# Optimization experiments

Hardware: AMD Instinct MI355X
Metric: run time of the kernel (lower is better)

## Reference

```python
import jax, jax.numpy as jnp
import numpy as np

N_FREQ = 12
NUM_LODS = 8
NUM_SAMPLED_LODS = 1
N_NEURONS = 64
OUT_CH = 11  # NUM_CANONICAL_CHANNELS = sum([3,3,1,1,1,1,1])
LRELU_SLOPE = 0.01
B = 1 << 20
# base_res = max_resolution >> (n_levels - 1); fpl = save_bits // quantize_bits = 4
GRIDS = [dict(base_res=16, n_levels=8, fpl=4),   # max_res 2048
         dict(base_res=16, n_levels=7, fpl=4)]   # max_res 1024


def _level_geom(base_res, level):
    # tcnn dense grid: scale = base_res * 2^level - 1, res = ceil(scale) + 1
    scale = base_res * (2.0 ** level) - 1.0
    res = int(np.ceil(scale)) + 1
    return res, scale


def _grid_n_params(g):
    return sum(_level_geom(g['base_res'], l)[0] ** 2 for l in range(g['n_levels'])) * g['fpl']


def triangle_wave(uv, n_freq):
    # tcnn TriangleWave: per dim, per frequency f: tri(x * 2^f), dim-major layout
    freqs = (2.0 ** jnp.arange(n_freq, dtype=jnp.float32))
    xf = uv[:, :, None] * freqs                      # [B, 2, F]
    t = jnp.abs(xf - jnp.floor(xf + 0.5)) * 4.0 - 1.0
    return t.reshape(uv.shape[0], -1)                # [B, 2*F]


def dense_grid_encode(uv, params_flat, base_res, n_levels, fpl):
    # Multi-level dense grid with bilinear interpolation (tcnn Grid/Dense/Linear).
    feats = []
    offset = 0
    for level in range(n_levels):
        res, scale = _level_geom(base_res, level)
        n = res * res * fpl
        table = params_flat[offset:offset + n].reshape(res * res, fpl)
        offset += n
        pos = uv * scale + 0.5                       # [B, 2]
        p0f = jnp.floor(pos)
        w = pos - p0f                                # bilinear weights
        p0 = jnp.clip(p0f.astype(jnp.int32), 0, res - 1)
        p1 = jnp.minimum(p0 + 1, res - 1)
        ix0, iy0 = p0[:, 0], p0[:, 1]
        ix1, iy1 = p1[:, 0], p1[:, 1]
        # tcnn index stride: dim0 fastest -> idx = ix + iy*res
        f00 = table[iy0 * res + ix0]
        f10 = table[iy0 * res + ix1]
        f01 = table[iy1 * res + ix0]
        f11 = table[iy1 * res + ix1]
        wx = w[:, 0:1]
        wy = w[:, 1:2]
        f = (f00 * (1 - wx) + f10 * wx) * (1 - wy) + (f01 * (1 - wx) + f11 * wx) * wy
        feats.append(f)                              # [B, fpl]
    return jnp.concatenate(feats, axis=1)            # [B, n_levels*fpl], level-major


def _forward(x, grid0_params, grid1_params, W_in, W_h, W_out):
    uvs = jnp.remainder(x[:, 0:2], 1.0)
    lod = x[:, 2:3]
    mips = lod * (NUM_LODS - NUM_SAMPLED_LODS)       # [B, 1]
    pe = triangle_wave(uvs, N_FREQ)                  # [B, 24]
    feats = []
    for g, params in zip(GRIDS, [grid0_params, grid1_params]):
        L, F = g['n_levels'], g['fpl']
        allf = dense_grid_encode(uvs, params, g['base_res'], L, F)  # [B, L*F]
        clipped = jnp.minimum(mips, float(L - NUM_SAMPLED_LODS))
        cols = ((L - NUM_SAMPLED_LODS - clipped) * F
                + jnp.arange(F * NUM_SAMPLED_LODS, dtype=jnp.float32)).astype(jnp.int32)
        feats.append(jnp.take_along_axis(allf, cols, axis=1))       # [B, F]
    inp = jnp.concatenate([pe] + feats + [lod], axis=1)             # [B, 33]
    lrelu = lambda h: jnp.where(h > 0, h, LRELU_SLOPE * h)
    h = lrelu(inp @ W_in)
    h = lrelu(h @ W_h)
    return lrelu(h @ W_out)                          # [B, 11]


def setup_inputs() -> dict:
    key = jax.random.key(0)
    ks = jax.random.split(key, 6)
    x = jax.random.uniform(ks[0], (B, 3), dtype=jnp.float32)
    grid0 = jax.random.uniform(ks[1], (_grid_n_params(GRIDS[0]),), jnp.float32, -0.1, 0.1)
    grid1 = jax.random.uniform(ks[2], (_grid_n_params(GRIDS[1]),), jnp.float32, -0.1, 0.1)
    n_in = N_FREQ * 2 + sum(g['fpl'] for g in GRIDS) * NUM_SAMPLED_LODS + 1
    W_in = jax.random.normal(ks[3], (n_in, N_NEURONS), jnp.float32) / np.float32(np.sqrt(n_in))
    W_h = jax.random.normal(ks[4], (N_NEURONS, N_NEURONS), jnp.float32) / np.float32(np.sqrt(N_NEURONS))
    W_out = jax.random.normal(ks[5], (N_NEURONS, OUT_CH), jnp.float32) / np.float32(np.sqrt(N_NEURONS))
    return dict(x=x, grid0_params=grid0, grid1_params=grid1, W_in=W_in, W_h=W_h, W_out=W_out)


def reference(x, grid0_params, grid1_params, W_in, W_h, W_out):
    return _forward(x, grid0_params, grid1_params, W_in, W_h, W_out)
```

## Files before the change

### kernel.cpp

```cpp
#include <hip/hip_runtime.h>

typedef float f32x4 __attribute__((ext_vector_type(4)));
typedef __bf16 bf16x8 __attribute__((ext_vector_type(8)));

#define PERM __builtin_amdgcn_perm

static __device__ __forceinline__ bf16x8 as_bf(uint4 v) {
    union { uint4 u; bf16x8 b; } c; c.u = v; return c.b;
}

static __device__ __forceinline__ float lrelu(float x) { return x > 0.0f ? x : 0.01f * x; }

static __device__ __forceinline__ unsigned pack_hilo(float v) {
    unsigned b = __float_as_uint(v);
    unsigned hi = (b + 0x7FFFu + ((b >> 16) & 1u)) >> 16;
    float hif = __uint_as_float(hi << 16);
    float lof = v - hif;
    unsigned lb = __float_as_uint(lof);
    unsigned lo = (lb + 0x7FFFu + ((lb >> 16) & 1u)) >> 16;
    return (hi << 16) | lo;
}

static __device__ __forceinline__ void unpack_frag(uint4 p0, uint4 p1, uint4& hi, uint4& lo) {
    hi.x = PERM(p0.y, p0.x, 0x07060302u);
    hi.y = PERM(p0.w, p0.z, 0x07060302u);
    hi.z = PERM(p1.y, p1.x, 0x07060302u);
    hi.w = PERM(p1.w, p1.z, 0x07060302u);
    lo.x = PERM(p0.y, p0.x, 0x05040100u);
    lo.y = PERM(p0.w, p0.z, 0x05040100u);
    lo.z = PERM(p1.y, p1.x, 0x05040100u);
    lo.w = PERM(p1.w, p1.z, 0x05040100u);
}

static __device__ __forceinline__ void read_frag_w(const unsigned* q, uint4& hi, uint4& lo) {
    uint4 p0 = *(const uint4*)(q);
    uint4 p1 = *(const uint4*)(q + 4);
    unpack_frag(p0, p1, hi, lo);
}

static __device__ __forceinline__ void read_frag_a(const unsigned* actb, int r, int kbase, int g,
                                                   uint4& hi, uint4& lo) {
    const unsigned* row = actb + r * 64;
    int cb = (kbase >> 2) + 2 * g;
    int rx = r & 15;
    uint4 p0 = *(const uint4*)(row + ((cb ^ rx) << 2));
    uint4 p1 = *(const uint4*)(row + (((cb + 1) ^ rx) << 2));
    unpack_frag(p0, p1, hi, lo);
}

static __device__ __forceinline__ void act_store(unsigned* actb, int row, int col, unsigned val) {
    int pos = row * 64 + ((((col >> 2) ^ (row & 15)) << 2) | (col & 3));
    actb[pos] = val;
}

static __device__ __forceinline__ f32x4 mfma3(const uint4& ah, const uint4& al,
                                              const uint4& bh, const uint4& bl, f32x4 c) {
    c = __builtin_amdgcn_mfma_f32_16x16x32_bf16(as_bf(ah), as_bf(bh), c, 0, 0, 0);
    c = __builtin_amdgcn_mfma_f32_16x16x32_bf16(as_bf(al), as_bf(bh), c, 0, 0, 0);
    c = __builtin_amdgcn_mfma_f32_16x16x32_bf16(as_bf(ah), as_bf(bl), c, 0, 0, 0);
    return c;
}

static __device__ __forceinline__ void bilerp(const float4* __restrict__ tbl, float u, float v,
                                              int l, float out[4]) {
    const int res = 16 << l;
    const float scale = (float)(res - 1);
    float px = u * scale + 0.5f;
    float py = v * scale + 0.5f;
    float fx = floorf(px), fy = floorf(py);
    float wx = px - fx, wy = py - fy;
    int ix0 = min(max((int)fx, 0), res - 1);
    int iy0 = min(max((int)fy, 0), res - 1);
    int ix1 = min(ix0 + 1, res - 1);
    int iy1 = min(iy0 + 1, res - 1);
    unsigned base = (0x55555555u & ((1u << (2 * l)) - 1u)) * 256u;
    float4 f00 = tbl[base + iy0 * res + ix0];
    float4 f10 = tbl[base + iy0 * res + ix1];
    float4 f01 = tbl[base + iy1 * res + ix0];
    float4 f11 = tbl[base + iy1 * res + ix1];
    float owx = 1.0f - wx, owy = 1.0f - wy;
    out[0] = (f00.x * owx + f10.x * wx) * owy + (f01.x * owx + f11.x * wx) * wy;
    out[1] = (f00.y * owx + f10.y * wx) * owy + (f01.y * owx + f11.y * wx) * wy;
    out[2] = (f00.z * owx + f10.z * wx) * owy + (f01.z * owx + f11.z * wx) * wy;
    out[3] = (f00.w * owx + f10.w * wx) * owy + (f01.w * owx + f11.w * wx) * wy;
}

static __device__ __forceinline__ void grid_select(const float4* __restrict__ tbl, float u, float v,
                                                   float mips, float Lm1, float out[4]) {
    float clipped = fminf(mips, Lm1);
    float c0 = (Lm1 - clipped) * 4.0f;
    asm volatile("" : "+v"(c0));
    int col0 = (int)c0;
    int col1 = (int)(c0 + 1.0f);
    int col2 = (int)(c0 + 2.0f);
    int col3 = (int)(c0 + 3.0f);
    int lA = col0 >> 2;
    int lB = col3 >> 2;
    float A[4], Bv[4];
    bilerp(tbl, u, v, lA, A);
    bilerp(tbl, u, v, lB, Bv);
    int cols[4] = {col0, col1, col2, col3};
    #pragma unroll
    for (int j = 0; j < 4; ++j) {
        int lj = cols[j] >> 2;
        int fj = cols[j] & 3;
        float va = A[0];
        va = (fj == 1) ? A[1] : va;
        va = (fj == 2) ? A[2] : va;
        va = (fj == 3) ? A[3] : va;
        float vb = Bv[0];
        vb = (fj == 1) ? Bv[1] : vb;
        vb = (fj == 2) ? Bv[2] : vb;
        vb = (fj == 3) ? Bv[3] : vb;
        out[j] = (lj == lA) ? va : vb;
    }
}

#define LDS_U32 (2048 + 4096 + 1024 + 64 + 128 + 8192)

__global__ __launch_bounds__(256, 2) void tcnn_fwd(
    const float* __restrict__ x,
    const float4* __restrict__ g0,
    const float4* __restrict__ g1,
    const float* __restrict__ Win,
    const float* __restrict__ Wh,
    const float* __restrict__ Wout,
    float* __restrict__ out,
    int npts)
{
    extern __shared__ unsigned smem[];
    unsigned* s_winT  = smem;
    unsigned* s_whT   = s_winT + 2048;
    unsigned* s_woutT = s_whT + 4096;
    float*    s_lodw  = (float*)(s_woutT + 1024);
    float*    s_lodv  = s_lodw + 64;
    unsigned* s_act   = (unsigned*)(s_lodv + 128);

    const int tid = threadIdx.x;

    for (int e = tid; e < 2048; e += 256) {
        int n = e >> 5, k = e & 31;
        s_winT[n * 32 + k] = pack_hilo(Win[k * 64 + n]);
    }
    for (int e = tid; e < 4096; e += 256) {
        int n = e >> 6, k = e & 63;
        s_whT[n * 64 + k] = pack_hilo(Wh[k * 64 + n]);
    }
    for (int e = tid; e < 1024; e += 256) {
        int n = e >> 6, k = e & 63;
        float w = (n < 11) ? Wout[k * 11 + n] : 0.0f;
        s_woutT[n * 64 + k] = pack_hilo(w);
    }
    if (tid < 64) s_lodw[tid] = Win[32 * 64 + tid];
    __syncthreads();

    const int wv = tid >> 6;
    const int l = tid & 63;
    const int g = l >> 4;
    const int m = l & 15;
    const int half = l >> 5;
    const int p = l & 31;

    unsigned* act = s_act + wv * 2048;
    float* lodv = s_lodv + wv * 32;

    uint4 w1h[4], w1l[4];
    #pragma unroll
    for (int Nt = 0; Nt < 4; ++Nt)
        read_frag_w(s_winT + (Nt * 16 + m) * 32 + 8 * g, w1h[Nt], w1l[Nt]);
    uint4 w2h[4][2], w2l[4][2];
    #pragma unroll
    for (int Nt = 0; Nt < 4; ++Nt)
        #pragma unroll
        for (int ks = 0; ks < 2; ++ks)
            read_frag_w(s_whT + (Nt * 16 + m) * 64 + ks * 32 + 8 * g, w2h[Nt][ks], w2l[Nt][ks]);
    uint4 w3h[2], w3l[2];
    #pragma unroll
    for (int ks = 0; ks < 2; ++ks)
        read_frag_w(s_woutT + m * 64 + ks * 32 + 8 * g, w3h[ks], w3l[ks]);

    for (int cb = (blockIdx.x * 4 + wv) * 32; cb + 31 < npts; cb += gridDim.x * 128) {
        int gp = cb + p;
        float xu = x[gp * 3 + 0];
        float xv = x[gp * 3 + 1];
        float xl = x[gp * 3 + 2];
        float u = xu - floorf(xu);
        float vv = xv - floorf(xv);
        float coord = half ? vv : u;
        #pragma unroll
        for (int f = 0; f < 12; ++f) {
            float fr = (float)(1 << f);
            float xf = coord * fr;
            float t = fabsf(xf - floorf(xf + 0.5f)) * 4.0f - 1.0f;
            act_store(act, p, half * 12 + f, pack_hilo(t));
        }
        {
            const float4* tbl = half ? g1 : g0;
            float Lm1 = half ? 6.0f : 7.0f;
            float mips = xl * 7.0f;
            float gf[4];
            grid_select(tbl, u, vv, mips, Lm1, gf);
            #pragma unroll
            for (int j = 0; j < 4; ++j)
                act_store(act, p, 24 + half * 4 + j, pack_hilo(gf[j]));
        }
        if (half) lodv[p] = xl;
        __builtin_amdgcn_wave_barrier();

        uint4 a1h[2], a1l[2];
        #pragma unroll
        for (int Mt = 0; Mt < 2; ++Mt)
            read_frag_a(act, Mt * 16 + m, 0, g, a1h[Mt], a1l[Mt]);
        f32x4 acc1[2][4];
        #pragma unroll
        for (int Mt = 0; Mt < 2; ++Mt)
            #pragma unroll
            for (int Nt = 0; Nt < 4; ++Nt)
                acc1[Mt][Nt] = (f32x4){0.f, 0.f, 0.f, 0.f};
        #pragma unroll
        for (int Nt = 0; Nt < 4; ++Nt)
            #pragma unroll
            for (int Mt = 0; Mt < 2; ++Mt)
                acc1[Mt][Nt] = mfma3(a1h[Mt], a1l[Mt], w1h[Nt], w1l[Nt], acc1[Mt][Nt]);
        float lv[2][4];
        #pragma unroll
        for (int Mt = 0; Mt < 2; ++Mt)
            #pragma unroll
            for (int i = 0; i < 4; ++i)
                lv[Mt][i] = lodv[Mt * 16 + 4 * g + i];
        #pragma unroll
        for (int Nt = 0; Nt < 4; ++Nt) {
            float wl = s_lodw[Nt * 16 + m];
            #pragma unroll
            for (int Mt = 0; Mt < 2; ++Mt)
                #pragma unroll
                for (int i = 0; i < 4; ++i)
                    acc1[Mt][Nt][i] = fmaf(lv[Mt][i], wl, acc1[Mt][Nt][i]);
        }
        __builtin_amdgcn_wave_barrier();
        #pragma unroll
        for (int Mt = 0; Mt < 2; ++Mt)
            #pragma unroll
            for (int Nt = 0; Nt < 4; ++Nt)
                #pragma unroll
                for (int i = 0; i < 4; ++i)
                    act_store(act, Mt * 16 + 4 * g + i, Nt * 16 + m,
                              pack_hilo(lrelu(acc1[Mt][Nt][i])));
        __builtin_amdgcn_wave_barrier();

        f32x4 acc2[2][4];
        #pragma unroll
        for (int Mt = 0; Mt < 2; ++Mt)
            #pragma unroll
            for (int Nt = 0; Nt < 4; ++Nt)
                acc2[Mt][Nt] = (f32x4){0.f, 0.f, 0.f, 0.f};
        #pragma unroll
        for (int Mt = 0; Mt < 2; ++Mt) {
            uint4 ah[2], al[2];
            #pragma unroll
            for (int ks = 0; ks < 2; ++ks)
                read_frag_a(act, Mt * 16 + m, ks * 32, g, ah[ks], al[ks]);
            #pragma unroll
            for (int Nt = 0; Nt < 4; ++Nt)
                #pragma unroll
                for (int ks = 0; ks < 2; ++ks)
                    acc2[Mt][Nt] = mfma3(ah[ks], al[ks], w2h[Nt][ks], w2l[Nt][ks], acc2[Mt][Nt]);
        }
        __builtin_amdgcn_wave_barrier();
        #pragma unroll
        for (int Mt = 0; Mt < 2; ++Mt)
            #pragma unroll
            for (int Nt = 0; Nt < 4; ++Nt)
                #pragma unroll
                for (int i = 0; i < 4; ++i)
                    act_store(act, Mt * 16 + 4 * g + i, Nt * 16 + m,
                              pack_hilo(lrelu(acc2[Mt][Nt][i])));
        __builtin_amdgcn_wave_barrier();

        f32x4 acc3[2];
        acc3[0] = (f32x4){0.f, 0.f, 0.f, 0.f};
        acc3[1] = (f32x4){0.f, 0.f, 0.f, 0.f};
        #pragma unroll
        for (int Mt = 0; Mt < 2; ++Mt) {
            uint4 ah[2], al[2];
            #pragma unroll
            for (int ks = 0; ks < 2; ++ks)
                read_frag_a(act, Mt * 16 + m, ks * 32, g, ah[ks], al[ks]);
            #pragma unroll
            for (int ks = 0; ks < 2; ++ks)
                acc3[Mt] = mfma3(ah[ks], al[ks], w3h[ks], w3l[ks], acc3[Mt]);
        }
        #pragma unroll
        for (int Mt = 0; Mt < 2; ++Mt)
            #pragma unroll
            for (int i = 0; i < 4; ++i) {
                int row = Mt * 16 + 4 * g + i;
                float val = lrelu(acc3[Mt][i]);
                if (m < 11) out[(size_t)(cb + row) * 11 + m] = val;
            }
        __builtin_amdgcn_wave_barrier();
    }
}

extern "C" void kernel_launch(void* const* d_in, const int* in_sizes, int n_in,
                              void* d_out, int out_size, void* d_ws, size_t ws_size,
                              hipStream_t stream) {
    const float* x = (const float*)d_in[0];
    const float4* g0 = (const float4*)d_in[1];
    const float4* g1 = (const float4*)d_in[2];
    const float* Win = (const float*)d_in[3];
    const float* Wh = (const float*)d_in[4];
    const float* Wout = (const float*)d_in[5];
    float* out = (float*)d_out;
    int npts = in_sizes[0] / 3;
    tcnn_fwd<<<512, 256, LDS_U32 * 4, stream>>>(x, g0, g1, Win, Wh, Wout, out, npts);
}
```

Before: 275.7 us.

## Software-pipeline grid gathers for next tile behind current tile's MLP MFMAs

Splits the grid lookup into an issue phase (load eight float4 table entries) and a finish phase (bilinear blend). Inside the persistent loop, the x loads, gathers and positional encoding for the next 32-point tile are issued after the first MFMA layer of the current tile and consumed at the end of the iteration. This hides gather latency behind the matrix work. In exchange, the eight float4s and the packed features stay live across the MLP, raising register pressure under the 2-blocks-per-SM launch bound.

New measurement: 306.4 us. +11.1%, slower.

```diff
diff --git a/kernel.cpp b/kernel.cpp
--- a/kernel.cpp
+++ b/kernel.cpp
@@ -61,45 +61,59 @@
     return c;
 }
 
-static __device__ __forceinline__ void bilerp(const float4* __restrict__ tbl, float u, float v,
-                                              int l, float out[4]) {
+static __device__ __forceinline__ void issue_level(const float4* __restrict__ tbl, float u, float v,
+                                                   int l, float4 r[4], float& wx, float& wy) {
     const int res = 16 << l;
     const float scale = (float)(res - 1);
     float px = u * scale + 0.5f;
     float py = v * scale + 0.5f;
     float fx = floorf(px), fy = floorf(py);
-    float wx = px - fx, wy = py - fy;
+    wx = px - fx; wy = py - fy;
     int ix0 = min(max((int)fx, 0), res - 1);
     int iy0 = min(max((int)fy, 0), res - 1);
     int ix1 = min(ix0 + 1, res - 1);
     int iy1 = min(iy0 + 1, res - 1);
     unsigned base = (0x55555555u & ((1u << (2 * l)) - 1u)) * 256u;
-    float4 f00 = tbl[base + iy0 * res + ix0];
-    float4 f10 = tbl[base + iy0 * res + ix1];
-    float4 f01 = tbl[base + iy1 * res + ix0];
-    float4 f11 = tbl[base + iy1 * res + ix1];
-    float owx = 1.0f - wx, owy = 1.0f - wy;
-    out[0] = (f00.x * owx + f10.x * wx) * owy + (f01.x * owx + f11.x * wx) * wy;
-    out[1] = (f00.y * owx + f10.y * wx) * owy + (f01.y * owx + f11.y * wx) * wy;
-    out[2] = (f00.z * owx + f10.z * wx) * owy + (f01.z * owx + f11.z * wx) * wy;
-    out[3] = (f00.w * owx + f10.w * wx) * owy + (f01.w * owx + f11.w * wx) * wy;
-}
-
-static __device__ __forceinline__ void grid_select(const float4* __restrict__ tbl, float u, float v,
-                                                   float mips, float Lm1, float out[4]) {
+    r[0] = tbl[base + iy0 * res + ix0];
+    r[1] = tbl[base + iy0 * res + ix1];
+    r[2] = tbl[base + iy1 * res + ix0];
+    r[3] = tbl[base + iy1 * res + ix1];
+}
+
+static __device__ __forceinline__ void gather_issue(const float4* __restrict__ tbl, float u, float v,
+                                                    float mips, float Lm1,
+                                                    float4 r[8], float w[4], int cols[4]) {
     float clipped = fminf(mips, Lm1);
     float c0 = (Lm1 - clipped) * 4.0f;
     asm volatile("" : "+v"(c0));
-    int col0 = (int)c0;
-    int col1 = (int)(c0 + 1.0f);
-    int col2 = (int)(c0 + 2.0f);
-    int col3 = (int)(c0 + 3.0f);
-    int lA = col0 >> 2;
-    int lB = col3 >> 2;
+    cols[0] = (int)c0;
+    cols[1] = (int)(c0 + 1.0f);
+    cols[2] = (int)(c0 + 2.0f);
+    cols[3] = (int)(c0 + 3.0f);
+    int lA = cols[0] >> 2;
+    int lB = cols[3] >> 2;
+    issue_level(tbl, u, v, lA, &r[0], w[0], w[1]);
+    issue_level(tbl, u, v, lB, &r[4], w[2], w[3]);
+}
+
+static __device__ __forceinline__ void gather_finish(const float4 r[8], const float w[4],
+                                                     const int cols[4], float out[4]) {
     float A[4], Bv[4];
-    bilerp(tbl, u, v, lA, A);
-    bilerp(tbl, u, v, lB, Bv);
-    int cols[4] = {col0, col1, col2, col3};
+    {
+        float owx = 1.0f - w[0], owy = 1.0f - w[1];
+        A[0] = (r[0].x * owx + r[1].x * w[0]) * owy + (r[2].x * owx + r[3].x * w[0]) * w[1];
+        A[1] = (r[0].y * owx + r[1].y * w[0]) * owy + (r[2].y * owx + r[3].y * w[0]) * w[1];
+        A[2] = (r[0].z * owx + r[1].z * w[0]) * owy + (r[2].z * owx + r[3].z * w[0]) * w[1];
+        A[3] = (r[0].w * owx + r[1].w * w[0]) * owy + (r[2].w * owx + r[3].w * w[0]) * w[1];
+    }
+    {
+        float owx = 1.0f - w[2], owy = 1.0f - w[3];
+        Bv[0] = (r[4].x * owx + r[5].x * w[2]) * owy + (r[6].x * owx + r[7].x * w[2]) * w[3];
+        Bv[1] = (r[4].y * owx + r[5].y * w[2]) * owy + (r[6].y * owx + r[7].y * w[2]) * w[3];
+        Bv[2] = (r[4].z * owx + r[5].z * w[2]) * owy + (r[6].z * owx + r[7].z * w[2]) * w[3];
+        Bv[3] = (r[4].w * owx + r[5].w * w[2]) * owy + (r[6].w * owx + r[7].w * w[2]) * w[3];
+    }
+    int lA = cols[0] >> 2;
     #pragma unroll
     for (int j = 0; j < 4; ++j) {
         int lj = cols[j] >> 2;
@@ -113,6 +127,16 @@
         vb = (fj == 2) ? Bv[2] : vb;
         vb = (fj == 3) ? Bv[3] : vb;
         out[j] = (lj == lA) ? va : vb;
+    }
+}
+
+static __device__ __forceinline__ void pe_compute(float coord, unsigned pep[12]) {
+    #pragma unroll
+    for (int f = 0; f < 12; ++f) {
+        float fr = (float)(1 << f);
+        float xf = coord * fr;
+        float t = fabsf(xf - floorf(xf + 0.5f)) * 4.0f - 1.0f;
+        pep[f] = pack_hilo(t);
     }
 }
 
@@ -179,32 +203,45 @@
     for (int ks = 0; ks < 2; ++ks)
         read_frag_w(s_woutT + m * 64 + ks * 32 + 8 * g, w3h[ks], w3l[ks]);
 
-    for (int cb = (blockIdx.x * 4 + wv) * 32; cb + 31 < npts; cb += gridDim.x * 128) {
-        int gp = cb + p;
+    const float4* __restrict__ mytbl = half ? g1 : g0;
+    const float myLm1 = half ? 6.0f : 7.0f;
+    const int STRIDE = gridDim.x * 128;
+
+    int cb0 = (blockIdx.x * 4 + wv) * 32;
+    if (cb0 + 31 >= npts) return;
+
+    unsigned pep[12], gfp[4];
+    float lodcur;
+    {
+        int gp = cb0 + p;
         float xu = x[gp * 3 + 0];
         float xv = x[gp * 3 + 1];
         float xl = x[gp * 3 + 2];
         float u = xu - floorf(xu);
         float vv = xv - floorf(xv);
-        float coord = half ? vv : u;
-        #pragma unroll
-        for (int f = 0; f < 12; ++f) {
-            float fr = (float)(1 << f);
-            float xf = coord * fr;
-            float t = fabsf(xf - floorf(xf + 0.5f)) * 4.0f - 1.0f;
-            act_store(act, p, half * 12 + f, pack_hilo(t));
-        }
-        {
-            const float4* tbl = half ? g1 : g0;
-            float Lm1 = half ? 6.0f : 7.0f;
-            float mips = xl * 7.0f;
-            float gf[4];
-            grid_select(tbl, u, vv, mips, Lm1, gf);
-            #pragma unroll
-            for (int j = 0; j < 4; ++j)
-                act_store(act, p, 24 + half * 4 + j, pack_hilo(gf[j]));
-        }
-        if (half) lodv[p] = xl;
+        pe_compute(half ? vv : u, pep);
+        float4 r[8]; float wgt[4]; int cols[4];
+        gather_issue(mytbl, u, vv, xl * 7.0f, myLm1, r, wgt, cols);
+        float gf[4];
+        gather_finish(r, wgt, cols, gf);
+        #pragma unroll
+        for (int j = 0; j < 4; ++j) gfp[j] = pack_hilo(gf[j]);
+        lodcur = xl;
+    }
+
+    for (int cb = cb0; cb + 31 < npts; cb += STRIDE) {
+        int next_cb = cb + STRIDE;
+        if (next_cb + 31 >= npts) next_cb = cb;
+        int gpn = next_cb + p;
+        float xun = x[gpn * 3 + 0];
+        float xvn = x[gpn * 3 + 1];
+        float xln = x[gpn * 3 + 2];
+
+        #pragma unroll
+        for (int f = 0; f < 12; ++f) act_store(act, p, half * 12 + f, pep[f]);
+        #pragma unroll
+        for (int j = 0; j < 4; ++j) act_store(act, p, 24 + half * 4 + j, gfp[j]);
+        if (half) lodv[p] = lodcur;
         __builtin_amdgcn_wave_barrier();
 
         uint4 a1h[2], a1l[2];
@@ -222,6 +259,13 @@
             #pragma unroll
             for (int Mt = 0; Mt < 2; ++Mt)
                 acc1[Mt][Nt] = mfma3(a1h[Mt], a1l[Mt], w1h[Nt], w1l[Nt], acc1[Mt][Nt]);
+
+        float un = xun - floorf(xun);
+        float vvn = xvn - floorf(xvn);
+        float4 r[8]; float wgt[4]; int cols[4];
+        gather_issue(mytbl, un, vvn, xln * 7.0f, myLm1, r, wgt, cols);
+        pe_compute(half ? vvn : un, pep);
+
         float lv[2][4];
         #pragma unroll
         for (int Mt = 0; Mt < 2; ++Mt)
@@ -299,6 +343,12 @@
                 if (m < 11) out[(size_t)(cb + row) * 11 + m] = val;
             }
         __builtin_amdgcn_wave_barrier();
+
+        float gf[4];
+        gather_finish(r, wgt, cols, gf);
+        #pragma unroll
+        for (int j = 0; j < 4; ++j) gfp[j] = pack_hilo(gf[j]);
+        lodcur = xln;
     }
 }
 
```
